# Optimization experiments

Hardware: AMD Instinct MI355X
Metric: run time of the kernel (lower is better)

## Reference

```python
import jax, jax.numpy as jnp
import numpy as np

B, L, H, NH = 8, 384, 512, 8
DH = H // NH
MAX_SEQ_LEN = 384


def setup_inputs() -> dict:
    key = jax.random.key(0)
    ks = jax.random.split(key, 16)
    s = 0.02
    seq_len = jnp.concatenate([
        jnp.array([L], dtype=jnp.int32),
        jax.random.randint(ks[3], (B - 1,), L // 2, L + 1, dtype=jnp.int32),
    ])
    return {
        "key": jax.random.normal(ks[0], (B, L, H), jnp.float32),
        "query": jax.random.normal(ks[1], (B, L, H), jnp.float32),
        "value": jax.random.normal(ks[2], (B, L, H), jnp.float32),
        "seq_len": seq_len,
        "pe": jax.random.normal(ks[4], (2 * MAX_SEQ_LEN + 1, H), jnp.float32) * s,
        "Wk": jax.random.normal(ks[5], (H, H), jnp.float32) * s,
        "bk": jnp.zeros((H,), jnp.float32),
        "Wq": jax.random.normal(ks[6], (H, H), jnp.float32) * s,
        "bq": jnp.zeros((H,), jnp.float32),
        "Wv": jax.random.normal(ks[7], (H, H), jnp.float32) * s,
        "bv": jnp.zeros((H,), jnp.float32),
        "Wr": jax.random.normal(ks[8], (H, H), jnp.float32) * s,
        "br": jnp.zeros((H,), jnp.float32),
        "u_bias": jax.random.normal(ks[9], (NH, DH), jnp.float32) * s,
        "v_bias": jax.random.normal(ks[10], (NH, DH), jnp.float32) * s,
        "Wff": jax.random.normal(ks[11], (H, H), jnp.float32) * s,
        "bff": jnp.zeros((H,), jnp.float32),
    }


def reference(key, query, value, seq_len, pe, Wk, bk, Wq, bq, Wv, bv, Wr, br, u_bias, v_bias, Wff, bff):
    # relative distances: rel[i, j] = j - i, in [-(L-1), L-1]
    rel = jnp.arange(L)[None, :] - jnp.arange(L)[:, None]          # [L, L]
    rpe = pe[rel + MAX_SEQ_LEN]                                    # [L, L, H]

    k = (key @ Wk.T + bk).reshape(B, L, NH, DH)
    q = (query @ Wq.T + bq).reshape(B, L, NH, DH)
    v = (value @ Wv.T + bv).reshape(B, L, NH, DH)
    rpe = (rpe @ Wr.T + br).reshape(L, L, NH, DH)

    # Transformer-XL score terms
    A = jnp.einsum('bihd,bjhd->bhij', q, k)                        # content-content
    Bt = jnp.einsum('bihd,ijhd->bhij', q, rpe)                     # content-position
    C = jnp.einsum('hd,bjhd->bhj', u_bias, k)[:, :, None, :]       # global content bias
    Dt = jnp.einsum('hd,ijhd->hij', v_bias, rpe)[None]             # global position bias

    scores = (A + Bt + C + Dt) / jnp.sqrt(jnp.float32(DH))
    key_mask = jnp.arange(L)[None, :] < seq_len[:, None]           # [B, L]
    scores = jnp.where(key_mask[:, None, None, :], scores, -1e15)
    attn = jax.nn.softmax(scores, axis=-1)                         # [B, NH, L, L]

    out = jnp.einsum('bhij,bjhd->bihd', attn, v).reshape(B, L, H)
    return out @ Wff.T + bff
```

## Files before the change

kernel.cpp:

```cpp
#include <hip/hip_runtime.h>

#define B_  8
#define L_  384
#define H_  512
#define NH_ 8
#define DH_ 64
#define RRM 768

typedef short bf16x8 __attribute__((ext_vector_type(8)));
typedef float f32x4  __attribute__((ext_vector_type(4)));
typedef unsigned int u32;
typedef u32 u32x4 __attribute__((ext_vector_type(4)));
#define MFMA_BF16 __builtin_amdgcn_mfma_f32_16x16x32_bf16

static __device__ __forceinline__ unsigned short f2bf(float f) {
    unsigned u = __builtin_bit_cast(unsigned, f);
    u += 0x7fffu + ((u >> 16) & 1u);
    return (unsigned short)(u >> 16);
}
static __device__ __forceinline__ float bf2f(unsigned short s) {
    unsigned u = ((unsigned)s) << 16;
    return __builtin_bit_cast(float, u);
}
static __device__ __forceinline__ u32 pk2(float lo, float hi) {
    u32 r;
    asm("v_cvt_pk_bf16_f32 %0, %1, %2" : "=v"(r) : "v"(lo), "v"(hi));
    return r;
}
static __device__ __forceinline__ void glds16(const void* g, void* l) {
    __builtin_amdgcn_global_load_lds(
        (const __attribute__((address_space(1))) u32*)g,
        (__attribute__((address_space(3))) u32*)l, 16, 0, 0);
}

struct WCvtArgs { const float* src[5]; unsigned short* dst[5]; };
__global__ __launch_bounds__(256) void cvt_w(WCvtArgs a) {
    const int gid = blockIdx.x * 256 + threadIdx.x;
    const int m = gid >> 15;
    const int rem = gid & 32767;
    const int row = rem >> 6, c = rem & 63;
    const int kc = c >> 3, sjd = c & 7;
    const int sjs = sjd ^ (row & 7);
    const float* s = a.src[m] + row * 512 + kc * 64 + sjs * 8;
    const f32x4 v0 = *(const f32x4*)s;
    const f32x4 v1 = *(const f32x4*)(s + 4);
    u32x4 o;
    o[0] = pk2(v0[0], v0[1]);
    o[1] = pk2(v0[2], v0[3]);
    o[2] = pk2(v1[0], v1[1]);
    o[3] = pk2(v1[2], v1[3]);
    *(u32x4*)(a.dst[m] + row * 512 + kc * 64 + sjd * 8) = o;
}

template <bool IS_FF>
__global__ __launch_bounds__(256) void gemm_nt(
    const float* __restrict__ A0, const float* __restrict__ A1,
    const float* __restrict__ A2, const float* __restrict__ A3,
    const unsigned short* __restrict__ Abf,
    const unsigned short* __restrict__ W0, const unsigned short* __restrict__ W1,
    const unsigned short* __restrict__ W2, const unsigned short* __restrict__ W3,
    const unsigned short* __restrict__ W4,
    const float* __restrict__ b0, const float* __restrict__ b1,
    const float* __restrict__ b2, const float* __restrict__ b3,
    const float* __restrict__ b4,
    const float* __restrict__ ub, const float* __restrict__ vbias,
    unsigned short* __restrict__ qu, unsigned short* __restrict__ qv,
    unsigned short* __restrict__ kb, unsigned short* __restrict__ vT,
    unsigned short* __restrict__ rp, float* __restrict__ ff) {

    const int z = IS_FF ? 4 : blockIdx.z;
    if (!IS_FF && z == 3 && blockIdx.y >= 12) return;
    const float* Af   = z == 0 ? A0 : z == 1 ? A1 : z == 2 ? A2 : A3;
    const unsigned short* Wb =
        z == 0 ? W0 : z == 1 ? W1 : z == 2 ? W2 : z == 3 ? W3 : W4;
    const float* bias = z == 0 ? b0 : z == 1 ? b1 : z == 2 ? b2 : z == 3 ? b3 : b4;

    __shared__ __align__(16) unsigned short AsF[2 * 64 * 64];
    __shared__ __align__(16) unsigned short BsF[2 * 128 * 64];

    const int tid = threadIdx.x;
    const int w = tid >> 6, lane = tid & 63;
    const int quad = lane >> 4, lm = lane & 15;
    const int wr = (w & 1) * 32;
    const int wc = (w >> 1) * 64;

    const int sr = lane >> 3, sj = lane & 7;
    const size_t aoff = (size_t)(blockIdx.y * 64 + w * 16 + sr) * 512 + sj * 8;
    const unsigned short* gB =
        Wb + (size_t)(blockIdx.x * 128 + w * 32 + sr) * 512 + sj * 8;

    f32x4 la[2][2];
    bf16x8 lah[2];

    auto LOAD_A = [&](int kc) {
        #pragma unroll
        for (int t = 0; t < 2; ++t) {
            if constexpr (IS_FF) {
                lah[t] = *(const bf16x8*)(Abf + aoff + t * 8 * 512 + kc * 64);
            } else {
                const float* p = Af + aoff + t * 8 * 512 + kc * 64;
                la[t][0] = *(const f32x4*)p;
                la[t][1] = *(const f32x4*)(p + 4);
            }
        }
    };
    auto WRITE_A = [&](int buf) {
        #pragma unroll
        for (int t = 0; t < 2; ++t) {
            const int off = buf * 4096 + (w * 16 + t * 8 + sr) * 64 + (sj ^ sr) * 8;
            if constexpr (IS_FF) {
                *(bf16x8*)&AsF[off] = lah[t];
            } else {
                u32x4 pa;
                pa[0] = pk2(la[t][0][0], la[t][0][1]);
                pa[1] = pk2(la[t][0][2], la[t][0][3]);
                pa[2] = pk2(la[t][1][0], la[t][1][1]);
                pa[3] = pk2(la[t][1][2], la[t][1][3]);
                *(u32x4*)&AsF[off] = pa;
            }
        }
    };
    auto STAGE_B = [&](int kc, int buf) {
        #pragma unroll
        for (int t = 0; t < 4; ++t) {
            int off = buf * 8192 + (w * 32 + t * 8) * 64;
            off = __builtin_amdgcn_readfirstlane(off);
            glds16(gB + t * 8 * 512 + kc * 64, &BsF[off]);
        }
    };

    f32x4 acc[2][4] = {};
    LOAD_A(0);
    for (int kc = 0; kc < 8; ++kc) {
        const int buf = kc & 1;
        WRITE_A(buf);
        STAGE_B(kc, buf);
        if (kc < 7) LOAD_A(kc + 1);
        __syncthreads();
        const int ba = buf * 4096, bb = buf * 8192;
        #pragma unroll
        for (int ks = 0; ks < 2; ++ks) {
            const int s = (((ks * 4 + quad) ^ (lm & 7))) * 8;
            bf16x8 a0 = *(const bf16x8*)&AsF[ba + (wr + lm) * 64 + s];
            bf16x8 a1 = *(const bf16x8*)&AsF[ba + (wr + 16 + lm) * 64 + s];
            bf16x8 w0 = *(const bf16x8*)&BsF[bb + (wc + lm) * 64 + s];
            bf16x8 w1 = *(const bf16x8*)&BsF[bb + (wc + 16 + lm) * 64 + s];
            bf16x8 w2 = *(const bf16x8*)&BsF[bb + (wc + 32 + lm) * 64 + s];
            bf16x8 w3 = *(const bf16x8*)&BsF[bb + (wc + 48 + lm) * 64 + s];
            acc[0][0] = MFMA_BF16(a0, w0, acc[0][0], 0, 0, 0);
            acc[0][1] = MFMA_BF16(a0, w1, acc[0][1], 0, 0, 0);
            acc[0][2] = MFMA_BF16(a0, w2, acc[0][2], 0, 0, 0);
            acc[0][3] = MFMA_BF16(a0, w3, acc[0][3], 0, 0, 0);
            acc[1][0] = MFMA_BF16(a1, w0, acc[1][0], 0, 0, 0);
            acc[1][1] = MFMA_BF16(a1, w1, acc[1][1], 0, 0, 0);
            acc[1][2] = MFMA_BF16(a1, w2, acc[1][2], 0, 0, 0);
            acc[1][3] = MFMA_BF16(a1, w3, acc[1][3], 0, 0, 0);
        }
        __syncthreads();
    }

    #pragma unroll
    for (int si = 0; si < 2; ++si) {
        #pragma unroll
        for (int sj2 = 0; sj2 < 4; ++sj2) {
            #pragma unroll
            for (int reg = 0; reg < 4; ++reg) {
                const int r = blockIdx.y * 64 + wr + si * 16 + quad * 4 + reg;
                const int c = blockIdx.x * 128 + wc + sj2 * 16 + lm;
                const float val = acc[si][sj2][reg] + bias[c];
                if (IS_FF) {
                    ff[r * 512 + c] = val;
                } else if (z == 0) {
                    const int bb2 = r / L_, ii = r - bb2 * L_;
                    const int h = c >> 6, d = c & 63;
                    const int idx = ((bb2 * NH_ + h) * L_ + ii) * DH_ + d;
                    qu[idx] = f2bf((val + ub[c]) * 0.125f);
                    qv[idx] = f2bf((val + vbias[c]) * 0.125f);
                } else if (z == 1) {
                    const int bb2 = r / L_, ii = r - bb2 * L_;
                    const int h = c >> 6, d = c & 63;
                    kb[((bb2 * NH_ + h) * L_ + ii) * DH_ + d] = f2bf(val);
                } else if (z == 2) {
                    const int bb2 = r / L_, ii = r - bb2 * L_;
                    const int h = c >> 6, d = c & 63;
                    vT[((bb2 * NH_ + h) * DH_ + d) * L_ + ii] = f2bf(val);
                } else {
                    rp[r * 512 + c] = f2bf(val);
                }
            }
        }
    }
}

#define BTSTR 424
__global__ __launch_bounds__(256) void attn_fused(
    const unsigned short* __restrict__ qu, const unsigned short* __restrict__ qv,
    const unsigned short* __restrict__ kbf, const unsigned short* __restrict__ vT,
    const unsigned short* __restrict__ rp, const int* __restrict__ seq_len,
    unsigned short* __restrict__ Obf) {
    __shared__ __align__(16) unsigned short BtP[32 * BTSTR];
    __shared__ float mx_red[32][2];
    __shared__ float sm_red[32][2];
    const int lane = threadIdx.x & 63, wv = threadIdx.x >> 6;
    const int quad = lane >> 4, lm = lane & 15;
    const int bh = blockIdx.y, b = bh >> 3, h = bh & 7;
    const int i0 = blockIdx.x * 32;
    const int sl = seq_len[b];
    const int msub = wv & 1, nh = wv >> 1;
    const int m_lo = 353 - i0;
    const int i_fr = i0 + msub * 16 + lm;

    {
        const unsigned short* qvr = qv + (size_t)(bh * L_ + i_fr) * DH_;
        const bf16x8 av0 = *(const bf16x8*)(qvr + quad * 8);
        const bf16x8 av1 = *(const bf16x8*)(qvr + 32 + quad * 8);
        #pragma unroll
        for (int ns = 0; ns < 13; ++ns) {
            const int ntl = nh * 208 + ns * 16;
            if (ntl <= sl + 30) {
                const int n = ntl + lm;
                const unsigned short* rrow = rp + (size_t)(m_lo + n) * 512 + h * 64;
                f32x4 bacc = {};
                bacc = MFMA_BF16(av0, *(const bf16x8*)(rrow + quad * 8), bacc, 0, 0, 0);
                bacc = MFMA_BF16(av1, *(const bf16x8*)(rrow + 32 + quad * 8), bacc, 0, 0, 0);
                #pragma unroll
                for (int reg = 0; reg < 4; ++reg) {
                    const int il = msub * 16 + quad * 4 + reg;
                    BtP[il * BTSTR + n] = f2bf(bacc[reg]);
                }
            }
        }
    }
    const unsigned short* qur = qu + (size_t)(bh * L_ + i_fr) * DH_;
    const bf16x8 au0 = *(const bf16x8*)(qur + quad * 8);
    const bf16x8 au1 = *(const bf16x8*)(qur + 32 + quad * 8);
    __syncthreads();

    f32x4 sc[12];
    #pragma unroll
    for (int ns = 0; ns < 12; ++ns) {
        const int jt = nh * 192 + ns * 16;
        if (jt < sl) {
            const unsigned short* krow = kbf + (size_t)(bh * L_ + jt + lm) * DH_;
            f32x4 a = {};
            a = MFMA_BF16(au0, *(const bf16x8*)(krow + quad * 8), a, 0, 0, 0);
            a = MFMA_BF16(au1, *(const bf16x8*)(krow + 32 + quad * 8), a, 0, 0, 0);
            sc[ns] = a;
        } else {
            sc[ns] = f32x4{-1e30f, -1e30f, -1e30f, -1e30f};
        }
    }
    const int jbase = nh * 192 + lm;
    #pragma unroll
    for (int ns = 0; ns < 12; ++ns) {
        const int j = jbase + ns * 16;
        #pragma unroll
        for (int reg = 0; reg < 4; ++reg) {
            const int il = msub * 16 + quad * 4 + reg;
            float val = -1e30f;
            if (j < sl) val = sc[ns][reg] + bf2f(BtP[il * BTSTR + (j - il + 31)]);
            sc[ns][reg] = val;
        }
    }

    const int il0 = msub * 16 + quad * 4;
    float mx4[4], sm4[4], inv4[4];
    #pragma unroll
    for (int reg = 0; reg < 4; ++reg) {
        float m = sc[0][reg];
        #pragma unroll
        for (int ns = 1; ns < 12; ++ns) m = fmaxf(m, sc[ns][reg]);
        #pragma unroll
        for (int o = 1; o < 16; o <<= 1) m = fmaxf(m, __shfl_xor(m, o));
        mx4[reg] = m;
    }
    if (lm == 0) {
        #pragma unroll
        for (int reg = 0; reg < 4; ++reg) mx_red[il0 + reg][nh] = mx4[reg];
    }
    __syncthreads();
    #pragma unroll
    for (int reg = 0; reg < 4; ++reg)
        mx4[reg] = fmaxf(mx_red[il0 + reg][0], mx_red[il0 + reg][1]);
    #pragma unroll
    for (int reg = 0; reg < 4; ++reg) sm4[reg] = 0.f;
    #pragma unroll
    for (int ns = 0; ns < 12; ++ns) {
        #pragma unroll
        for (int reg = 0; reg < 4; ++reg) {
            const float e = __expf(sc[ns][reg] - mx4[reg]);
            sc[ns][reg] = e;
            sm4[reg] += e;
        }
    }
    #pragma unroll
    for (int reg = 0; reg < 4; ++reg) {
        float s = sm4[reg];
        #pragma unroll
        for (int o = 1; o < 16; o <<= 1) s += __shfl_xor(s, o);
        sm4[reg] = s;
    }
    if (lm == 0) {
        #pragma unroll
        for (int reg = 0; reg < 4; ++reg) sm_red[il0 + reg][nh] = sm4[reg];
    }
    __syncthreads();
    #pragma unroll
    for (int reg = 0; reg < 4; ++reg)
        inv4[reg] = 1.f / (sm_red[il0 + reg][0] + sm_red[il0 + reg][1]);

    #pragma unroll
    for (int ns = 0; ns < 12; ++ns) {
        const int j = jbase + ns * 16;
        #pragma unroll
        for (int reg = 0; reg < 4; ++reg)
            BtP[(il0 + reg) * BTSTR + j] = f2bf(sc[ns][reg] * inv4[reg]);
    }
    __syncthreads();

    {
        const int pr = msub * 16 + lm;
        const int nkc = (sl + 31) >> 5;
        f32x4 oacc[2] = {};
        for (int kc = 0; kc < nkc; ++kc) {
            const bf16x8 af = *(const bf16x8*)&BtP[pr * BTSTR + kc * 32 + quad * 8];
            #pragma unroll
            for (int t = 0; t < 2; ++t) {
                const int n = nh * 32 + t * 16 + lm;
                const unsigned short* vrow = vT + (size_t)(bh * DH_ + n) * L_ + kc * 32 + quad * 8;
                oacc[t] = MFMA_BF16(af, *(const bf16x8*)(vrow), oacc[t], 0, 0, 0);
            }
        }
        #pragma unroll
        for (int t = 0; t < 2; ++t) {
            #pragma unroll
            for (int reg = 0; reg < 4; ++reg) {
                const int i = i0 + msub * 16 + quad * 4 + reg;
                const int d = nh * 32 + t * 16 + lm;
                Obf[(size_t)(b * L_ + i) * H_ + h * DH_ + d] = f2bf(oacc[t][reg]);
            }
        }
    }
}

extern "C" void kernel_launch(void* const* d_in, const int* in_sizes, int n_in,
                              void* d_out, int out_size, void* d_ws, size_t ws_size,
                              hipStream_t stream) {
    const float* key    = (const float*)d_in[0];
    const float* query  = (const float*)d_in[1];
    const float* value  = (const float*)d_in[2];
    const int*   seqlen = (const int*)d_in[3];
    const float* pe     = (const float*)d_in[4];
    const float* Wk     = (const float*)d_in[5];
    const float* bk     = (const float*)d_in[6];
    const float* Wq     = (const float*)d_in[7];
    const float* bq     = (const float*)d_in[8];
    const float* Wv     = (const float*)d_in[9];
    const float* bv     = (const float*)d_in[10];
    const float* Wr     = (const float*)d_in[11];
    const float* br     = (const float*)d_in[12];
    const float* u_bias = (const float*)d_in[13];
    const float* v_bias = (const float*)d_in[14];
    const float* Wff    = (const float*)d_in[15];
    const float* bff    = (const float*)d_in[16];

    const size_t nTok = (size_t)B_ * L_ * H_;
    const size_t nPe  = (size_t)RRM * H_;
    const size_t nW   = (size_t)H_ * H_;
    unsigned short* p  = (unsigned short*)d_ws;
    unsigned short* qu   = p; p += nTok;
    unsigned short* qv   = p; p += nTok;
    unsigned short* kb   = p; p += nTok;
    unsigned short* vT   = p; p += nTok;
    unsigned short* rp   = p; p += nPe + 512;
    unsigned short* Obf  = p; p += nTok;
    unsigned short* Wqb  = p; p += nW;
    unsigned short* Wkb  = p; p += nW;
    unsigned short* Wvb  = p; p += nW;
    unsigned short* Wrb  = p; p += nW;
    unsigned short* Wffb = p; p += nW;

    WCvtArgs wa;
    wa.src[0] = Wq;  wa.dst[0] = Wqb;
    wa.src[1] = Wk;  wa.dst[1] = Wkb;
    wa.src[2] = Wv;  wa.dst[2] = Wvb;
    wa.src[3] = Wr;  wa.dst[3] = Wrb;
    wa.src[4] = Wff; wa.dst[4] = Wffb;
    cvt_w<<<640, 256, 0, stream>>>(wa);

    gemm_nt<false><<<dim3(4, 48, 4), 256, 0, stream>>>(
         query, key, value, pe,  nullptr,
         Wqb, Wkb, Wvb, Wrb, nullptr,
         bq, bk, bv, br, nullptr,
         u_bias, v_bias,
         qu, qv, kb, vT, rp,
         nullptr);

    attn_fused<<<dim3(L_ / 32, B_ * NH_), 256, 0, stream>>>(
        qu, qv, kb, vT, rp, seqlen, Obf);

    gemm_nt<true><<<dim3(4, 48, 1), 256, 0, stream>>>(
         nullptr, nullptr, nullptr, nullptr,  Obf,
         nullptr, nullptr, nullptr, nullptr, Wffb,
         nullptr, nullptr, nullptr, nullptr, bff,
         nullptr, nullptr,
         nullptr, nullptr, nullptr, nullptr, nullptr,
         (float*)d_out);
}
```

Baseline: 152.3 us.

## Remap workgroups XCD-aware, flatten grids, drop redundant trailing barrier

All three kernels now launch 1-D grids and remap blockIdx so that consecutive logical tiles land on the same XCD (blockIdx & 7). The aim is better L2 reuse of shared weight and activation tiles within each chiplet. The projection GEMM grid also shrinks from 768 to 624 blocks, so the empty rpe-tail blocks that used to exit early are no longer launched. The second __syncthreads per K step is removed, which relies on double buffering plus the first barrier to keep LDS reuse safe.

```diff
diff --git a/kernel.cpp b/kernel.cpp
--- a/kernel.cpp
+++ b/kernel.cpp
@@ -68,8 +68,17 @@
     unsigned short* __restrict__ kb, unsigned short* __restrict__ vT,
     unsigned short* __restrict__ rp, float* __restrict__ ff) {
 
-    const int z = IS_FF ? 4 : blockIdx.z;
-    if (!IS_FF && z == 3 && blockIdx.y >= 12) return;
+    int bx, by, z;
+    if constexpr (IS_FF) {
+        const int wg = (blockIdx.x & 7) * 24 + (blockIdx.x >> 3);
+        bx = wg & 3; by = wg >> 2; z = 4;
+    } else {
+        const int wg = (blockIdx.x & 7) * 78 + (blockIdx.x >> 3);
+        bx = wg & 3;
+        const int t = wg >> 2;
+        z  = t < 144 ? t / 48 : 3;
+        by = t < 144 ? t % 48 : t - 144;
+    }
     const float* Af   = z == 0 ? A0 : z == 1 ? A1 : z == 2 ? A2 : A3;
     const unsigned short* Wb =
         z == 0 ? W0 : z == 1 ? W1 : z == 2 ? W2 : z == 3 ? W3 : W4;
@@ -85,47 +94,47 @@
     const int wc = (w >> 1) * 64;
 
     const int sr = lane >> 3, sj = lane & 7;
-    const size_t aoff = (size_t)(blockIdx.y * 64 + w * 16 + sr) * 512 + sj * 8;
+    const size_t aoff = (size_t)(by * 64 + w * 16 + sr) * 512 + sj * 8;
     const unsigned short* gB =
-        Wb + (size_t)(blockIdx.x * 128 + w * 32 + sr) * 512 + sj * 8;
+        Wb + (size_t)(bx * 128 + w * 32 + sr) * 512 + sj * 8;
 
     f32x4 la[2][2];
     bf16x8 lah[2];
 
     auto LOAD_A = [&](int kc) {
         #pragma unroll
-        for (int t = 0; t < 2; ++t) {
+        for (int t2 = 0; t2 < 2; ++t2) {
             if constexpr (IS_FF) {
-                lah[t] = *(const bf16x8*)(Abf + aoff + t * 8 * 512 + kc * 64);
+                lah[t2] = *(const bf16x8*)(Abf + aoff + t2 * 8 * 512 + kc * 64);
             } else {
-                const float* p = Af + aoff + t * 8 * 512 + kc * 64;
-                la[t][0] = *(const f32x4*)p;
-                la[t][1] = *(const f32x4*)(p + 4);
+                const float* p = Af + aoff + t2 * 8 * 512 + kc * 64;
+                la[t2][0] = *(const f32x4*)p;
+                la[t2][1] = *(const f32x4*)(p + 4);
             }
         }
     };
     auto WRITE_A = [&](int buf) {
         #pragma unroll
-        for (int t = 0; t < 2; ++t) {
-            const int off = buf * 4096 + (w * 16 + t * 8 + sr) * 64 + (sj ^ sr) * 8;
+        for (int t2 = 0; t2 < 2; ++t2) {
+            const int off = buf * 4096 + (w * 16 + t2 * 8 + sr) * 64 + (sj ^ sr) * 8;
             if constexpr (IS_FF) {
-                *(bf16x8*)&AsF[off] = lah[t];
+                *(bf16x8*)&AsF[off] = lah[t2];
             } else {
                 u32x4 pa;
-                pa[0] = pk2(la[t][0][0], la[t][0][1]);
-                pa[1] = pk2(la[t][0][2], la[t][0][3]);
-                pa[2] = pk2(la[t][1][0], la[t][1][1]);
-                pa[3] = pk2(la[t][1][2], la[t][1][3]);
+                pa[0] = pk2(la[t2][0][0], la[t2][0][1]);
+                pa[1] = pk2(la[t2][0][2], la[t2][0][3]);
+                pa[2] = pk2(la[t2][1][0], la[t2][1][1]);
+                pa[3] = pk2(la[t2][1][2], la[t2][1][3]);
                 *(u32x4*)&AsF[off] = pa;
             }
         }
     };
     auto STAGE_B = [&](int kc, int buf) {
         #pragma unroll
-        for (int t = 0; t < 4; ++t) {
-            int off = buf * 8192 + (w * 32 + t * 8) * 64;
+        for (int t2 = 0; t2 < 4; ++t2) {
+            int off = buf * 8192 + (w * 32 + t2 * 8) * 64;
             off = __builtin_amdgcn_readfirstlane(off);
-            glds16(gB + t * 8 * 512 + kc * 64, &BsF[off]);
+            glds16(gB + t2 * 8 * 512 + kc * 64, &BsF[off]);
         }
     };
 
@@ -156,7 +165,6 @@
             acc[1][2] = MFMA_BF16(a1, w2, acc[1][2], 0, 0, 0);
             acc[1][3] = MFMA_BF16(a1, w3, acc[1][3], 0, 0, 0);
         }
-        __syncthreads();
     }
 
     #pragma unroll
@@ -165,8 +173,8 @@
         for (int sj2 = 0; sj2 < 4; ++sj2) {
             #pragma unroll
             for (int reg = 0; reg < 4; ++reg) {
-                const int r = blockIdx.y * 64 + wr + si * 16 + quad * 4 + reg;
-                const int c = blockIdx.x * 128 + wc + sj2 * 16 + lm;
+                const int r = by * 64 + wr + si * 16 + quad * 4 + reg;
+                const int c = bx * 128 + wc + sj2 * 16 + lm;
                 const float val = acc[si][sj2][reg] + bias[c];
                 if (IS_FF) {
                     ff[r * 512 + c] = val;
@@ -203,8 +211,9 @@
     __shared__ float sm_red[32][2];
     const int lane = threadIdx.x & 63, wv = threadIdx.x >> 6;
     const int quad = lane >> 4, lm = lane & 15;
-    const int bh = blockIdx.y, b = bh >> 3, h = bh & 7;
-    const int i0 = blockIdx.x * 32;
+    const int wg = (blockIdx.x & 7) * 96 + (blockIdx.x >> 3);
+    const int bh = wg / 12, b = bh >> 3, h = bh & 7;
+    const int i0 = (wg % 12) * 32;
     const int sl = seq_len[b];
     const int msub = wv & 1, nh = wv >> 1;
     const int m_lo = 353 - i0;
@@ -388,7 +397,7 @@
     wa.src[4] = Wff; wa.dst[4] = Wffb;
     cvt_w<<<640, 256, 0, stream>>>(wa);
 
-    gemm_nt<false><<<dim3(4, 48, 4), 256, 0, stream>>>(
+    gemm_nt<false><<<dim3(624), 256, 0, stream>>>(
          query, key, value, pe,  nullptr,
          Wqb, Wkb, Wvb, Wrb, nullptr,
          bq, bk, bv, br, nullptr,
@@ -396,10 +405,10 @@
          qu, qv, kb, vT, rp,
          nullptr);
 
-    attn_fused<<<dim3(L_ / 32, B_ * NH_), 256, 0, stream>>>(
+    attn_fused<<<dim3(768), 256, 0, stream>>>(
         qu, qv, kb, vT, rp, seqlen, Obf);
 
-    gemm_nt<true><<<dim3(4, 48, 1), 256, 0, stream>>>(
+    gemm_nt<true><<<dim3(192), 256, 0, stream>>>(
          nullptr, nullptr, nullptr, nullptr,  Obf,
          nullptr, nullptr, nullptr, nullptr, Wffb,
          nullptr, nullptr, nullptr, nullptr, bff,
```

Measured after the change: 159.7 us. 4.9% more time.
